# Kernel optimization log

Hardware: AMD Instinct MI355X
Metric: run time of the kernel (lower is better)

## Reference

```python
import jax, jax.numpy as jnp
import numpy as np

INPUT_DIM = 28
HIDDEN_DIM = 128
OUTPUT_DIM = 10


def setup_inputs() -> dict:
    key = jax.random.key(0)
    ks = jax.random.split(key, 7)
    B, T = 4096, 512
    std = 1.0 / np.sqrt(HIDDEN_DIM)

    def u(k, shape):
        return jax.random.uniform(k, shape, jnp.float32, -std, std)

    x = jax.random.normal(ks[0], (B, T, INPUT_DIM), jnp.float32)
    # gate order g=0: reset(r), g=1: update(z), g=2: new(n)
    w_x = u(ks[1], (3, INPUT_DIM, HIDDEN_DIM))
    b_x = u(ks[2], (3, HIDDEN_DIM))
    w_h = u(ks[3], (3, HIDDEN_DIM, HIDDEN_DIM))
    b_h = u(ks[4], (3, HIDDEN_DIM))
    fc_w = u(ks[5], (HIDDEN_DIM, OUTPUT_DIM))
    fc_b = u(ks[6], (OUTPUT_DIM,))
    return {"x": x, "w_x": w_x, "b_x": b_x, "w_h": w_h, "b_h": b_h,
            "fc_w": fc_w, "fc_b": fc_b}


def gru_last_hidden(x, w_x, b_x, w_h, b_h):
    B, T, _ = x.shape
    # Precompute input projections for all gates/timesteps: [T, 3, B, H]
    gx = jnp.einsum('bti,gih->tgbh', x, w_x) + b_x[None, :, None, :]
    h0 = jnp.zeros((B, HIDDEN_DIM), x.dtype)

    def step(h, gx_t):
        gh = jnp.einsum('bh,gho->gbo', h, w_h) + b_h[:, None, :]  # [3, B, H]
        r = jax.nn.sigmoid(gx_t[0] + gh[0])
        z = jax.nn.sigmoid(gx_t[1] + gh[1])
        n = jnp.tanh(gx_t[2] + r * gh[2])
        h_next = (1.0 - z) * n + z * h
        return h_next, None

    h_last, _ = jax.lax.scan(step, h0, gx)
    return h_last


def reference(x, w_x, b_x, w_h, b_h, fc_w, fc_b):
    h_last = gru_last_hidden(x, w_x, b_x, w_h, b_h)  # [B, H]
    return h_last @ fc_w + fc_b  # [B, OUTPUT_DIM]
```

## Files before the change

### kernel.cpp

```cpp
#include <hip/hip_runtime.h>

#define T_STEPS 512
#define IN_DIM 28
#define HDIM 128
#define BT 16
#define NTHREADS 512

typedef _Float16 f16x8 __attribute__((ext_vector_type(8)));
typedef float f32x4 __attribute__((ext_vector_type(4)));

#if __has_builtin(__builtin_amdgcn_exp2f)
#define EXP2F __builtin_amdgcn_exp2f
#else
#define EXP2F exp2f
#endif
#if __has_builtin(__builtin_amdgcn_rcpf)
#define RCPF __builtin_amdgcn_rcpf
#else
#define RCPF(v) (1.0f / (v))
#endif

__device__ __forceinline__ float fast_sigmoid(float v) {
    return RCPF(1.0f + EXP2F(v * -1.442695041f));
}
__device__ __forceinline__ float fast_tanh(float v) {
    return 2.0f * RCPF(1.0f + EXP2F(v * -2.885390082f)) - 1.0f;
}

#define HB0 0
#define HB1 4096
#define XS0 8192
#define XS1 (8192 + 1024)

__global__ __launch_bounds__(NTHREADS, 2) void gru_fused(
    const float* __restrict__ x,
    const float* __restrict__ w_x,
    const float* __restrict__ b_x,
    const float* __restrict__ w_h,
    const float* __restrict__ b_h,
    const float* __restrict__ fc_w,
    const float* __restrict__ fc_b,
    float* __restrict__ out)
{
    const int tid = threadIdx.x;
    const int wv  = tid >> 6;
    const int l   = tid & 63;
    const int lr  = l & 15;
    const int lg  = l >> 4;
    const int b0  = blockIdx.x * BT;
    const int col = wv * 16 + lr;

    __shared__ __align__(16) unsigned char lds[2 * 4096 + 2 * 1024];

    f16x8 whf[3][4];
#pragma unroll
    for (int g = 0; g < 3; ++g)
#pragma unroll
        for (int kf = 0; kf < 4; ++kf)
#pragma unroll
            for (int e = 0; e < 8; ++e)
                whf[g][kf][e] = (_Float16)w_h[(g * HDIM + kf * 32 + lg * 8 + e) * HDIM + col];

    f16x8 wxf[3];
#pragma unroll
    for (int g = 0; g < 3; ++g)
#pragma unroll
        for (int e = 0; e < 8; ++e) {
            int k = lg * 8 + e;
            wxf[g][e] = (k < IN_DIM) ? (_Float16)w_x[(g * IN_DIM + k) * HDIM + col]
                                     : (_Float16)0.0f;
        }

    f32x4 zero4 = {0.0f, 0.0f, 0.0f, 0.0f};
    f32x4 cinitX2, cinitG[3];
    {
        float bx2 = b_x[2 * HDIM + col];
        cinitX2 = (f32x4){bx2, bx2, bx2, bx2};
        float s0 = b_h[0 * HDIM + col] + b_x[0 * HDIM + col];
        float s1 = b_h[1 * HDIM + col] + b_x[1 * HDIM + col];
        float s2 = b_h[2 * HDIM + col];
        cinitG[0] = (f32x4){s0, s0, s0, s0};
        cinitG[1] = (f32x4){s1, s1, s1, s1};
        cinitG[2] = (f32x4){s2, s2, s2, s2};
    }

    int ha_off[4];
#pragma unroll
    for (int kf = 0; kf < 4; ++kf)
        ha_off[kf] = (lr << 8) + (((kf << 6) + (lg << 4)) ^ ((lr & 7) << 4));
    int wa_off[4];
#pragma unroll
    for (int r = 0; r < 4; ++r) {
        int row = lg * 4 + r;
        wa_off[r] = (row << 8) + ((col << 1) ^ ((row & 7) << 4));
    }
    const int xr_off = lr * 64 + ((lg << 4) ^ ((lr & 3) << 4));

    const int  xrow_s  = tid >> 5;
    const int  xk      = tid & 31;
    const bool x_valid = (xk < IN_DIM);
    const int  xw_off  = xrow_s * 64 + ((xk << 1) ^ ((xrow_s & 3) << 4));
    const float* gptr  = x + (size_t)(b0 + xrow_s) * (T_STEPS * IN_DIM)
                           + (x_valid ? xk : 0);

    for (int i = tid; i < 1024; i += NTHREADS) ((int*)lds)[i] = 0;
    {
        float v0 = x_valid ? gptr[0] : 0.0f;
        *(_Float16*)(lds + XS0 + xw_off) = (_Float16)v0;
    }
    float h_c[4] = {0.0f, 0.0f, 0.0f, 0.0f};
    __syncthreads();

    auto step = [&](int t, int cur) {
        unsigned char* hcur = lds + (cur ? HB1 : HB0);
        unsigned char* hnxt = lds + (cur ? HB0 : HB1);
        unsigned char* xcur = lds + (cur ? XS1 : XS0);
        unsigned char* xnxt = lds + (cur ? XS0 : XS1);

        int   tn  = (t + 1 < T_STEPS) ? t + 1 : t;
        float xpf = x_valid ? gptr[(size_t)tn * IN_DIM] : 0.0f;

        f16x8 xa = *(const f16x8*)(xcur + xr_off);
        f16x8 ha[4];
#pragma unroll
        for (int kf = 0; kf < 4; ++kf)
            ha[kf] = *(const f16x8*)(hcur + ha_off[kf]);

        f32x4 accX[3];
        accX[0] = __builtin_amdgcn_mfma_f32_16x16x32_f16(xa, wxf[0], zero4, 0, 0, 0);
        accX[1] = __builtin_amdgcn_mfma_f32_16x16x32_f16(xa, wxf[1], zero4, 0, 0, 0);
        accX[2] = __builtin_amdgcn_mfma_f32_16x16x32_f16(xa, wxf[2], cinitX2, 0, 0, 0);

        f32x4 accG[3];
#pragma unroll
        for (int g = 0; g < 3; ++g)
            accG[g] = __builtin_amdgcn_mfma_f32_16x16x32_f16(ha[0], whf[g][0], cinitG[g], 0, 0, 0);
#pragma unroll
        for (int kf = 1; kf < 4; ++kf)
#pragma unroll
            for (int g = 0; g < 3; ++g)
                accG[g] = __builtin_amdgcn_mfma_f32_16x16x32_f16(ha[kf], whf[g][kf], accG[g], 0, 0, 0);

#pragma unroll
        for (int r = 0; r < 4; ++r) {
            float rg = fast_sigmoid(accX[0][r] + accG[0][r]);
            float zg = fast_sigmoid(accX[1][r] + accG[1][r]);
            float ng = fast_tanh(accX[2][r] + rg * accG[2][r]);
            h_c[r] = ng + zg * (h_c[r] - ng);
            *(_Float16*)(hnxt + wa_off[r]) = (_Float16)h_c[r];
        }

        *(_Float16*)(xnxt + xw_off) = (_Float16)xpf;

        __syncthreads();
    };

    for (int t = 0; t < T_STEPS; t += 2) {
        step(t, 0);
        step(t + 1, 1);
    }

    float* hf = (float*)lds;
#pragma unroll
    for (int r = 0; r < 4; ++r) hf[(lg * 4 + r) * HDIM + col] = h_c[r];
    __syncthreads();

    if (tid < BT * 10) {
        int b = tid / 10, o = tid % 10;
        float s = fc_b[o];
        for (int j = 0; j < HDIM; ++j) s += hf[b * HDIM + j] * fc_w[j * 10 + o];
        out[(size_t)(b0 + b) * 10 + o] = s;
    }
}

extern "C" void kernel_launch(void* const* d_in, const int* in_sizes, int n_in,
                              void* d_out, int out_size, void* d_ws, size_t ws_size,
                              hipStream_t stream) {
    const float* x    = (const float*)d_in[0];
    const float* w_x  = (const float*)d_in[1];
    const float* b_x  = (const float*)d_in[2];
    const float* w_h  = (const float*)d_in[3];
    const float* b_h  = (const float*)d_in[4];
    const float* fc_w = (const float*)d_in[5];
    const float* fc_b = (const float*)d_in[6];
    float* out = (float*)d_out;

    int B = in_sizes[0] / (T_STEPS * IN_DIM);
    gru_fused<<<B / BT, NTHREADS, 0, stream>>>(x, w_x, b_x, w_h, b_h, fc_w, fc_b, out);
}
```

Measured before the change: 787.7 us.

## Load x directly into MFMA fragments and pipeline input projection one step ahead

The input x is no longer staged through shared memory. Each lane loads its own 8 float elements with vector loads straight into the MFMA A-fragment, and the input-projection MFMAs for the next step are issued alongside the current recurrent MFMAs, so they sit off the critical path. The two sigmoid reciprocals are merged into one reciprocal of the product, and the h-buffer swizzle is changed. This removes the x LDS writes and reads, but it reads 8 floats per lane per step where 1 was read before, keeps extra live accumulator registers, and the shared reciprocal could overflow for large negative gate inputs.

Measured after the change: 675.2 us. 14.3% less time.

```diff
diff --git a/kernel.cpp b/kernel.cpp
--- a/kernel.cpp
+++ b/kernel.cpp
@@ -7,6 +7,7 @@
 #define NTHREADS 512
 
 typedef _Float16 f16x8 __attribute__((ext_vector_type(8)));
+typedef __fp16   fp16x2 __attribute__((ext_vector_type(2)));
 typedef float f32x4 __attribute__((ext_vector_type(4)));
 
 #if __has_builtin(__builtin_amdgcn_exp2f)
@@ -20,17 +21,16 @@
 #define RCPF(v) (1.0f / (v))
 #endif
 
-__device__ __forceinline__ float fast_sigmoid(float v) {
-    return RCPF(1.0f + EXP2F(v * -1.442695041f));
+#define SWZ(r) ((((r) + ((r) >> 3))) & 7)
+
+__device__ __forceinline__ f16x8 cvt_f16x8(f32x4 a, f32x4 b) {
+    union { f16x8 v; fp16x2 h[4]; } u;
+    u.h[0] = __builtin_amdgcn_cvt_pkrtz(a[0], a[1]);
+    u.h[1] = __builtin_amdgcn_cvt_pkrtz(a[2], a[3]);
+    u.h[2] = __builtin_amdgcn_cvt_pkrtz(b[0], b[1]);
+    u.h[3] = __builtin_amdgcn_cvt_pkrtz(b[2], b[3]);
+    return u.v;
 }
-__device__ __forceinline__ float fast_tanh(float v) {
-    return 2.0f * RCPF(1.0f + EXP2F(v * -2.885390082f)) - 1.0f;
-}
-
-#define HB0 0
-#define HB1 4096
-#define XS0 8192
-#define XS1 (8192 + 1024)
 
 __global__ __launch_bounds__(NTHREADS, 2) void gru_fused(
     const float* __restrict__ x,
@@ -50,7 +50,7 @@
     const int b0  = blockIdx.x * BT;
     const int col = wv * 16 + lr;
 
-    __shared__ __align__(16) unsigned char lds[2 * 4096 + 2 * 1024];
+    __shared__ __align__(16) unsigned char lds[2 * BT * HDIM * 2];
 
     f16x8 whf[3][4];
 #pragma unroll
@@ -71,7 +71,7 @@
                                      : (_Float16)0.0f;
         }
 
-    f32x4 zero4 = {0.0f, 0.0f, 0.0f, 0.0f};
+    const f32x4 zero4 = {0.0f, 0.0f, 0.0f, 0.0f};
     f32x4 cinitX2, cinitG[3];
     {
         float bx2 = b_x[2 * HDIM + col];
@@ -87,78 +87,89 @@
     int ha_off[4];
 #pragma unroll
     for (int kf = 0; kf < 4; ++kf)
-        ha_off[kf] = (lr << 8) + (((kf << 6) + (lg << 4)) ^ ((lr & 7) << 4));
+        ha_off[kf] = (lr << 8) + (((kf << 6) + (lg << 4)) ^ (SWZ(lr) << 4));
     int wa_off[4];
 #pragma unroll
     for (int r = 0; r < 4; ++r) {
         int row = lg * 4 + r;
-        wa_off[r] = (row << 8) + ((col << 1) ^ ((row & 7) << 4));
-    }
-    const int xr_off = lr * 64 + ((lg << 4) ^ ((lr & 3) << 4));
-
-    const int  xrow_s  = tid >> 5;
-    const int  xk      = tid & 31;
-    const bool x_valid = (xk < IN_DIM);
-    const int  xw_off  = xrow_s * 64 + ((xk << 1) ^ ((xrow_s & 3) << 4));
-    const float* gptr  = x + (size_t)(b0 + xrow_s) * (T_STEPS * IN_DIM)
-                           + (x_valid ? xk : 0);
-
-    for (int i = tid; i < 1024; i += NTHREADS) ((int*)lds)[i] = 0;
-    {
-        float v0 = x_valid ? gptr[0] : 0.0f;
-        *(_Float16*)(lds + XS0 + xw_off) = (_Float16)v0;
-    }
+        wa_off[r] = (row << 8) + ((col << 1) ^ (SWZ(row) << 4));
+    }
+
+    const float* xrow  = x + (size_t)(b0 + lr) * (T_STEPS * IN_DIM) + lg * 8;
+    const bool pad_hi  = (lg == 3);
+    const float* xrowh = xrow + (pad_hi ? 0 : 4);
+
+    for (int i = tid; i < BT * HDIM / 2; i += NTHREADS) ((int*)lds)[i] = 0;
+
+    f32x4 xlo = *(const f32x4*)(xrow);
+    f32x4 xhi = *(const f32x4*)(xrowh);
+    if (pad_hi) xhi = zero4;
+    f16x8 xa0 = cvt_f16x8(xlo, xhi);
+    f32x4 accXA[3], accXB[3];
+    accXA[0] = __builtin_amdgcn_mfma_f32_16x16x32_f16(xa0, wxf[0], zero4, 0, 0, 0);
+    accXA[1] = __builtin_amdgcn_mfma_f32_16x16x32_f16(xa0, wxf[1], zero4, 0, 0, 0);
+    accXA[2] = __builtin_amdgcn_mfma_f32_16x16x32_f16(xa0, wxf[2], cinitX2, 0, 0, 0);
+    xlo = *(const f32x4*)(xrow + IN_DIM);
+    xhi = *(const f32x4*)(xrowh + IN_DIM);
+
     float h_c[4] = {0.0f, 0.0f, 0.0f, 0.0f};
     __syncthreads();
 
-    auto step = [&](int t, int cur) {
-        unsigned char* hcur = lds + (cur ? HB1 : HB0);
-        unsigned char* hnxt = lds + (cur ? HB0 : HB1);
-        unsigned char* xcur = lds + (cur ? XS1 : XS0);
-        unsigned char* xnxt = lds + (cur ? XS0 : XS1);
-
-        int   tn  = (t + 1 < T_STEPS) ? t + 1 : t;
-        float xpf = x_valid ? gptr[(size_t)tn * IN_DIM] : 0.0f;
-
-        f16x8 xa = *(const f16x8*)(xcur + xr_off);
-        f16x8 ha[4];
-#pragma unroll
-        for (int kf = 0; kf < 4; ++kf)
-            ha[kf] = *(const f16x8*)(hcur + ha_off[kf]);
-
-        f32x4 accX[3];
-        accX[0] = __builtin_amdgcn_mfma_f32_16x16x32_f16(xa, wxf[0], zero4, 0, 0, 0);
-        accX[1] = __builtin_amdgcn_mfma_f32_16x16x32_f16(xa, wxf[1], zero4, 0, 0, 0);
-        accX[2] = __builtin_amdgcn_mfma_f32_16x16x32_f16(xa, wxf[2], cinitX2, 0, 0, 0);
-
-        f32x4 accG[3];
-#pragma unroll
-        for (int g = 0; g < 3; ++g)
-            accG[g] = __builtin_amdgcn_mfma_f32_16x16x32_f16(ha[0], whf[g][0], cinitG[g], 0, 0, 0);
-#pragma unroll
-        for (int kf = 1; kf < 4; ++kf)
-#pragma unroll
-            for (int g = 0; g < 3; ++g)
-                accG[g] = __builtin_amdgcn_mfma_f32_16x16x32_f16(ha[kf], whf[g][kf], accG[g], 0, 0, 0);
-
-#pragma unroll
-        for (int r = 0; r < 4; ++r) {
-            float rg = fast_sigmoid(accX[0][r] + accG[0][r]);
-            float zg = fast_sigmoid(accX[1][r] + accG[1][r]);
-            float ng = fast_tanh(accX[2][r] + rg * accG[2][r]);
-            h_c[r] = ng + zg * (h_c[r] - ng);
-            *(_Float16*)(hnxt + wa_off[r]) = (_Float16)h_c[r];
-        }
-
-        *(_Float16*)(xnxt + xw_off) = (_Float16)xpf;
-
-        __syncthreads();
-    };
+#define GRU_STEP(ACC_CUR, ACC_NXT, HCUR, HNXT, TPF)                               \
+    {                                                                              \
+        const unsigned char* hcur = lds + (HCUR);                                  \
+        unsigned char* hnxt = lds + (HNXT);                                        \
+        f16x8 ha[4];                                                               \
+        _Pragma("unroll")                                                          \
+        for (int kf = 0; kf < 4; ++kf)                                             \
+            ha[kf] = *(const f16x8*)(hcur + ha_off[kf]);                           \
+             \
+        f32x4 hi_m = pad_hi ? zero4 : xhi;                                         \
+        f16x8 xan = cvt_f16x8(xlo, hi_m);                                          \
+        {                                                                          \
+            int tp = (TPF); if (tp >= T_STEPS) tp = T_STEPS - 1;                   \
+            xlo = *(const f32x4*)(xrow + tp * IN_DIM);                             \
+            xhi = *(const f32x4*)(xrowh + tp * IN_DIM);                            \
+        }                                                                          \
+                        \
+        f32x4 accG[3];                                                             \
+        _Pragma("unroll")                                                          \
+        for (int g = 0; g < 3; ++g)                                                \
+            accG[g] = __builtin_amdgcn_mfma_f32_16x16x32_f16(ha[0], whf[g][0], cinitG[g], 0, 0, 0); \
+        _Pragma("unroll")                                                          \
+        for (int kf = 1; kf < 4; ++kf)                                             \
+            _Pragma("unroll")                                                      \
+            for (int g = 0; g < 3; ++g)                                            \
+                accG[g] = __builtin_amdgcn_mfma_f32_16x16x32_f16(ha[kf], whf[g][kf], accG[g], 0, 0, 0); \
+                  \
+        ACC_NXT[0] = __builtin_amdgcn_mfma_f32_16x16x32_f16(xan, wxf[0], zero4, 0, 0, 0);   \
+        ACC_NXT[1] = __builtin_amdgcn_mfma_f32_16x16x32_f16(xan, wxf[1], zero4, 0, 0, 0);   \
+        ACC_NXT[2] = __builtin_amdgcn_mfma_f32_16x16x32_f16(xan, wxf[2], cinitX2, 0, 0, 0); \
+          \
+        _Pragma("unroll")                                                          \
+        for (int r = 0; r < 4; ++r) {                                              \
+            float v0 = ACC_CUR[0][r] + accG[0][r];                                 \
+            float v1 = ACC_CUR[1][r] + accG[1][r];                                 \
+            float e0 = EXP2F(v0 * -1.442695041f);                                  \
+            float e1 = EXP2F(v1 * -1.442695041f);                                  \
+            float p0 = 1.0f + e0, p1 = 1.0f + e1;                                  \
+            float rd = RCPF(p0 * p1);                                              \
+            float rg = p1 * rd;                                   \
+            float zg = p0 * rd;                                   \
+            float q  = ACC_CUR[2][r] + rg * accG[2][r];                            \
+            float e2 = EXP2F(q * -2.885390082f);                                   \
+            float ng = 2.0f * RCPF(1.0f + e2) - 1.0f;                 \
+            h_c[r] = ng + zg * (h_c[r] - ng);                                      \
+            *(_Float16*)(hnxt + wa_off[r]) = (_Float16)h_c[r];                     \
+        }                                                                          \
+        __syncthreads();                                                           \
+    }
 
     for (int t = 0; t < T_STEPS; t += 2) {
-        step(t, 0);
-        step(t + 1, 1);
-    }
+        GRU_STEP(accXA, accXB, 0, 4096, t + 2)
+        GRU_STEP(accXB, accXA, 4096, 0, t + 3)
+    }
+#undef GRU_STEP
 
     float* hf = (float*)lds;
 #pragma unroll
```
